# Performance work log

Hardware: AMD Instinct MI355X
Metric: run time of the kernel (lower is better)

The kernel has to match this reference:

```python
import jax, jax.numpy as jnp
import numpy as np

# Synthetic base image encoder: patchify(16) -> Linear(768,768)+ReLU -> Linear(768,3072)+ReLU -> mean-pool -> Linear(3072,512)
B, T = 32, 8          # batch, num task vectors
D, DH, F, MH = 768, 3072, 512, 128  # patch dim, hidden, feat_dim, meta-net hidden


def _patchify(x):
    # x: [B,3,224,224] -> [B,196,768] (14x14 patches of 16x16x3)
    Bn = x.shape[0]
    p = x.reshape(Bn, 3, 14, 16, 14, 16).transpose(0, 2, 4, 1, 3, 5)
    return p.reshape(Bn, 196, 768)


def _encode_shared(p, W1, b1, W2, b2, W3, b3):
    h = jax.nn.relu(p @ W1 + b1)          # [B,196,768]
    h2 = jax.nn.relu(h @ W2 + b2)         # [B,196,3072]
    return h2.mean(axis=1) @ W3 + b3      # [B,512]


def setup_inputs() -> dict:
    key = jax.random.key(0)
    ks = jax.random.split(key, 18)
    inp = {"x": jax.random.normal(ks[0], (B, 3, 224, 224), jnp.float32)}
    shapes = {
        "W1": (D, D), "b1": (D,), "W2": (D, DH), "b2": (DH,), "W3": (DH, F), "b3": (F,),
        "dW1": (T, D, D), "db1": (T, D), "dW2": (T, D, DH), "db2": (T, DH),
        "dW3": (T, DH, F), "db3": (T, F),
        "mW1": (F, MH), "mb1": (MH,), "mW2": (MH, T), "mb2": (T,),
    }
    for i, (n, sh) in enumerate(shapes.items()):
        inp[n] = jax.random.normal(ks[i + 1], sh, jnp.float32) * 0.02
    return inp


def reference(x, W1, b1, W2, b2, W3, b3, dW1, db1, dW2, db2, dW3, db3, mW1, mb1, mW2, mb2):
    p = _patchify(x)
    # base features computed with frozen params (torch.no_grad -> stop_gradient)
    base = jax.lax.stop_gradient(_encode_shared(p, W1, b1, W2, b2, W3, b3))
    # MetaNet: Linear-ReLU-Linear -> per-sample task-vector coefficients [B,T]
    coefs = jax.nn.relu(base @ mW1 + mb1) @ mW2 + mb2
    # per-sample composed parameters: theta_b = theta + sum_t coef[b,t] * dtheta_t
    W1b = W1 + jnp.einsum('bt,tde->bde', coefs, dW1)   # [B,768,768]
    b1b = b1 + coefs @ db1
    W2b = W2 + jnp.einsum('bt,tde->bde', coefs, dW2)   # [B,768,3072]
    b2b = b2 + coefs @ db2
    W3b = W3 + jnp.einsum('bt,tdf->bdf', coefs, dW3)   # [B,3072,512]
    b3b = b3 + coefs @ db3
    # batched per-sample forward (replaces the python loop over the batch)
    h = jax.nn.relu(jnp.einsum('bpd,bde->bpe', p, W1b) + b1b[:, None, :])
    h2 = jax.nn.relu(jnp.einsum('bpe,bef->bpf', h, W2b) + b2b[:, None, :])
    return jnp.einsum('be,bef->bf', h2.mean(axis=1), W3b) + b3b  # [B,512]
```

## Files before the change

### kernel.cpp

```cpp
#include <hip/hip_runtime.h>
#include <hip/hip_bf16.h>

#define BATCH 32
#define NPATCH 196
#define PD 768
#define DH 3072
#define FD 512
#define MH 128
#define NT 8

typedef unsigned short u16;
typedef u16   u16x8  __attribute__((ext_vector_type(8)));
typedef short bf16x8 __attribute__((ext_vector_type(8)));
typedef float f32x4  __attribute__((ext_vector_type(4)));

__device__ __forceinline__ void async16(const void* g, void* l)
{
    __builtin_amdgcn_global_load_lds(
        (const __attribute__((address_space(1))) void*)g,
        (__attribute__((address_space(3))) void*)l, 16, 0, 0);
}

#define BARRIER() do { asm volatile("" ::: "memory"); __builtin_amdgcn_s_barrier(); asm volatile("" ::: "memory"); } while (0)
#define VMWAIT(n) asm volatile("s_waitcnt vmcnt(" #n ")" ::: "memory")

#define GK  768
#define NK  24
#define GBM 256
#define GBN 128
#define GBK 32
#define ASZ (GBM*GBK)
#define BSZ (GBN*GBK)

__global__ __launch_bounds__(512, 4)
void gemm_bf16(const u16* __restrict__ A, const u16* __restrict__ BT,
               const float* __restrict__ bias, u16* __restrict__ C,
               float* __restrict__ pooled,
               int M, int N, long sA, long sB, long sC, long sBias,
               int relu, int pool)
{
    const int z = blockIdx.z;
    A  += (long)z * sA;
    BT += (long)z * sB;
    C  += (long)z * sC;
    const float* bz = bias ? bias + (long)z * sBias : nullptr;

    __shared__ __align__(16) u16 As[3 * ASZ];
    __shared__ __align__(16) u16 Bs[3 * BSZ];

    const int tid  = threadIdx.x;
    const int lane = tid & 63;
    const int wave = tid >> 6;
    const int wr = (wave >> 1) * 64;
    const int wc = (wave & 1) * 64;
    const int m0 = blockIdx.y * GBM;
    const int n0 = blockIdx.x * GBN;
    const int lrow = lane & 15;
    const int koff = (lane >> 4) * 8;

    f32x4 acc[4][4] = {};

    auto issue = [&](int kt, int bi) {
        u16* asb = As + bi * ASZ;
        u16* bsb = Bs + bi * BSZ;
        const int k0 = kt * GBK;
#pragma unroll
        for (int r = 0; r < 2; ++r) {
            int chunk = r * 512 + tid;
            int row = chunk >> 2;
            int k8  = chunk & 3;
            int gm  = m0 + row; if (gm >= M) gm = M - 1;
            async16(A + (long)gm * GK + k0 + k8 * 8,
                    asb + (size_t)(r * 512 + wave * 64) * 8);
        }
        int rowb = tid >> 2;
        int k8b  = tid & 3;
        async16(BT + (long)(n0 + rowb) * GK + k0 + k8b * 8,
                bsb + (size_t)(wave * 64) * 8);
    };

    auto compute = [&](int bi) {
        const u16* asb = As + bi * ASZ;
        const u16* bsb = Bs + bi * BSZ;
        bf16x8 af[4], bfr[4];
#pragma unroll
        for (int i = 0; i < 4; ++i)
            af[i] = *(const bf16x8*)(asb + (wr + i * 16 + lrow) * GBK + koff);
#pragma unroll
        for (int j = 0; j < 4; ++j)
            bfr[j] = *(const bf16x8*)(bsb + (wc + j * 16 + lrow) * GBK + koff);
#pragma unroll
        for (int i = 0; i < 4; ++i)
#pragma unroll
            for (int j = 0; j < 4; ++j)
                acc[i][j] = __builtin_amdgcn_mfma_f32_16x16x32_bf16(af[i], bfr[j], acc[i][j], 0, 0, 0);
    };

    issue(0, 0); issue(1, 1); issue(2, 2);

    for (int ii = 0; ii < 7; ++ii) {
        int i0 = ii * 3;
        VMWAIT(6); BARRIER(); compute(0); BARRIER(); issue(i0 + 3, 0);
        VMWAIT(6); BARRIER(); compute(1); BARRIER(); issue(i0 + 4, 1);
        VMWAIT(6); BARRIER(); compute(2); BARRIER(); issue(i0 + 5, 2);
    }
    VMWAIT(6); BARRIER(); compute(0); BARRIER();
    VMWAIT(3); BARRIER(); compute(1); BARRIER();
    VMWAIT(0); BARRIER(); compute(2);

    const int crow = (lane >> 4) * 4;
    const int ccol = lane & 15;

    if (!pool) {
#pragma unroll
        for (int j = 0; j < 4; ++j) {
            int gn = n0 + wc + j * 16 + ccol;
            float bv = bz ? bz[gn] : 0.f;
#pragma unroll
            for (int i = 0; i < 4; ++i) {
#pragma unroll
                for (int rg = 0; rg < 4; ++rg) {
                    int gm = m0 + wr + i * 16 + crow + rg;
                    if (gm < M) {
                        float v = acc[i][j][rg] + bv;
                        if (relu) v = fmaxf(v, 0.f);
                        __hip_bfloat16 hv = __float2bfloat16(v);
                        C[(long)gm * N + gn] = *(u16*)&hv;
                    }
                }
            }
        }
    } else {
        float* poolbuf = (float*)As;
        __syncthreads();
        const int slot = (wave >> 1) * 4 + (lane >> 4);
#pragma unroll
        for (int j = 0; j < 4; ++j) {
            int gn = n0 + wc + j * 16 + ccol;
            float bv = bz ? bz[gn] : 0.f;
            float s = 0.f;
#pragma unroll
            for (int i = 0; i < 4; ++i) {
#pragma unroll
                for (int rg = 0; rg < 4; ++rg) {
                    int gm = wr + i * 16 + crow + rg;
                    if (gm < NPATCH) s += fmaxf(acc[i][j][rg] + bv, 0.f);
                }
            }
            poolbuf[slot * 128 + wc + j * 16 + ccol] = s;
        }
        __syncthreads();
        if (tid < 128) {
            float s = 0.f;
#pragma unroll
            for (int q = 0; q < 16; ++q) s += poolbuf[q * 128 + tid];
            pooled[(long)z * N + n0 + tid] = s * (1.0f / NPATCH);
        }
    }
}

#define SK_KC  64
#define SK_PAD 36

__global__ __launch_bounds__(256)
void skinny3(const float* __restrict__ A, const float* __restrict__ B0,
             const float* __restrict__ dB, const float* __restrict__ cf,
             float* __restrict__ partial)
{
    const int ks = blockIdx.x;
    const int z  = blockIdx.y;
    const int KS = gridDim.x;
    const int k0 = ks * SK_KC;
    const float* B = (z == 0) ? B0 : dB + (long)(z - 1) * DH * FD;

    __shared__ __align__(16) float Asl[SK_KC][SK_PAD];

    const int tid  = threadIdx.x;
    const int nthr = tid & 63;
    const int bg   = tid >> 6;
    const int n    = nthr * 8;

    for (int idx = tid; idx < 32 * SK_KC; idx += 256) {
        int b = idx >> 6;
        int k = idx & (SK_KC - 1);
        float sc = (z == 0) ? 1.f : cf[b * NT + (z - 1)];
        Asl[k][b] = sc * A[(long)b * DH + k0 + k];
    }
    __syncthreads();

    f32x4 acc[8][2] = {};
    for (int k = 0; k < SK_KC; ++k) {
        const float* bp = B + (long)(k0 + k) * FD + n;
        f32x4 w0 = *(const f32x4*)bp;
        f32x4 w1 = *(const f32x4*)(bp + 4);
        f32x4 a0 = *(const f32x4*)&Asl[k][bg * 8];
        f32x4 a1 = *(const f32x4*)&Asl[k][bg * 8 + 4];
#pragma unroll
        for (int q = 0; q < 4; ++q) {
#pragma unroll
            for (int c = 0; c < 4; ++c) {
                acc[q][0][c]     = fmaf(a0[q], w0[c], acc[q][0][c]);
                acc[q][1][c]     = fmaf(a0[q], w1[c], acc[q][1][c]);
                acc[4 + q][0][c] = fmaf(a1[q], w0[c], acc[4 + q][0][c]);
                acc[4 + q][1][c] = fmaf(a1[q], w1[c], acc[4 + q][1][c]);
            }
        }
    }
    float* P = partial + ((long)(z * KS + ks) * BATCH + bg * 8) * FD + n;
#pragma unroll
    for (int bb = 0; bb < 8; ++bb) {
        *(f32x4*)(P + (long)bb * FD)     = acc[bb][0];
        *(f32x4*)(P + (long)bb * FD + 4) = acc[bb][1];
    }
}

__global__ __launch_bounds__(256)
void reduce_partials(const float* __restrict__ partial, float* __restrict__ dst, int per)
{
    int i  = blockIdx.x * 256 + threadIdx.x;
    int p0 = blockIdx.y * per;
    float s = 0.f;
    for (int p = 0; p < per; ++p)
        s += partial[(long)(p0 + p) * (BATCH * FD) + i];
    atomicAdd(&dst[i], s);
}

__global__ void patchify_bf(const float* __restrict__ x, u16* __restrict__ p, int total)
{
    int i = blockIdx.x * blockDim.x + threadIdx.x;
    if (i >= total) return;
    int d = i % PD;
    int rest = i / PD;
    int patch = rest % NPATCH;
    int b = rest / NPATCH;
    int c = d >> 8;
    int r = (d >> 4) & 15;
    int s = d & 15;
    int pr = patch / 14;
    int pc = patch % 14;
    float v = x[((long)(b * 3 + c) * 224 + (pr * 16 + r)) * 224 + (pc * 16 + s)];
    __hip_bfloat16 hv = __float2bfloat16(v);
    p[i] = *(u16*)&hv;
}

__global__ __launch_bounds__(256)
void wtrans2(const float* __restrict__ W1, u16* __restrict__ o1,
             const float* __restrict__ W2, u16* __restrict__ o2)
{
    const float* W; u16* outp; int K, N, t;
    if (blockIdx.x < 576) { W = W1; outp = o1; K = PD; N = PD;  t = blockIdx.x; }
    else                  { W = W2; outp = o2; K = PD; N = DH;  t = blockIdx.x - 576; }
    int nt = N / 32;
    int k0 = (t / nt) * 32;
    int n0 = (t % nt) * 32;

    __shared__ float Ws[32][33];
    const int tid = threadIdx.x;
#pragma unroll
    for (int r = 0; r < 4; ++r) {
        int idx = tid + r * 256;
        int kk = idx >> 5, nn = idx & 31;
        Ws[kk][nn] = W[(long)(k0 + kk) * N + n0 + nn];
    }
    __syncthreads();
#pragma unroll
    for (int r = 0; r < 4; ++r) {
        int idx = tid + r * 256;
        int kk = idx & 31, nn = idx >> 5;
        __hip_bfloat16 hv = __float2bfloat16(Ws[kk][nn]);
        outp[(long)(n0 + nn) * K + k0 + kk] = *(u16*)&hv;
    }
}

__global__ __launch_bounds__(128)
void compose_w(const float* __restrict__ W, const float* __restrict__ dW,
               const float* __restrict__ cf, u16* __restrict__ out,
               int K, int N)
{
    __shared__ float Ws[9][32][32];
    const int tid = threadIdx.x;
    const int k0 = blockIdx.x * 32;
    const int n0 = blockIdx.y * 32;
    const long tKN = (long)K * N;

#pragma unroll
    for (int a = 0; a < 9; ++a) {
        const float* src = (a == 0) ? W : dW + (long)(a - 1) * tKN;
#pragma unroll
        for (int r = 0; r < 8; ++r) {
            int idx = tid + r * 128;
            int kk = idx >> 5, nn = idx & 31;
            Ws[a][kk][nn] = src[(long)(k0 + kk) * N + n0 + nn];
        }
    }
    __syncthreads();

    const int nn = tid >> 2;
    const int k8 = (tid & 3) * 8;
    float w0[8], d[NT][8];
#pragma unroll
    for (int q = 0; q < 8; ++q) w0[q] = Ws[0][k8 + q][nn];
#pragma unroll
    for (int t = 0; t < NT; ++t)
#pragma unroll
        for (int q = 0; q < 8; ++q) d[t][q] = Ws[t + 1][k8 + q][nn];

    for (int b = 0; b < BATCH; ++b) {
        float c8[NT];
#pragma unroll
        for (int t = 0; t < NT; ++t) c8[t] = cf[b * NT + t];
        u16x8 o;
#pragma unroll
        for (int q = 0; q < 8; ++q) {
            float v = w0[q];
#pragma unroll
            for (int t = 0; t < NT; ++t) v = fmaf(c8[t], d[t][q], v);
            __hip_bfloat16 hv = __float2bfloat16(v);
            o[q] = *(u16*)&hv;
        }
        *(u16x8*)(out + ((long)b * N + (n0 + nn)) * K + k0 + k8) = o;
    }
}

__global__ void compose_bias3(const float* __restrict__ b1, const float* __restrict__ db1,
                              const float* __restrict__ b2, const float* __restrict__ db2,
                              const float* __restrict__ b3, const float* __restrict__ db3,
                              const float* __restrict__ cf,
                              float* __restrict__ o1, float* __restrict__ o2,
                              float* __restrict__ o3)
{
    int i = blockIdx.x * blockDim.x + threadIdx.x;
    const int t1 = BATCH * PD, t2 = BATCH * (PD + DH);
    const float* bs; const float* db; float* o; int N, j;
    if (i < t1)      { bs = b1; db = db1; o = o1; N = PD; j = i; }
    else if (i < t2) { bs = b2; db = db2; o = o2; N = DH; j = i - t1; }
    else {
        j = i - t2;
        if (j >= BATCH * FD) return;
        bs = b3; db = db3; o = o3; N = FD;
    }
    int n = j % N, b = j / N;
    float v = bs[n];
#pragma unroll
    for (int t = 0; t < NT; ++t) v = fmaf(cf[b * NT + t], db[(long)t * N + n], v);
    o[j] = v;
}

__global__ void bias_init(const float* __restrict__ bsrc, float* __restrict__ out, int N)
{
    int i = blockIdx.x * blockDim.x + threadIdx.x;
    if (i >= BATCH * N) return;
    out[i] = bsrc[i % N];
}

__global__ __launch_bounds__(256)
void hid_kernel(const float* __restrict__ base, const float* __restrict__ mW1,
                const float* __restrict__ mb1, float* __restrict__ hid)
{
    int gw   = blockIdx.x * 4 + (threadIdx.x >> 6);
    int lane = threadIdx.x & 63;
    int b = gw >> 7;
    int n = gw & 127;
    float s = 0.f;
#pragma unroll
    for (int i = 0; i < FD / 64; ++i) {
        int k = i * 64 + lane;
        s = fmaf(base[b * FD + k], mW1[k * MH + n], s);
    }
#pragma unroll
    for (int off = 32; off; off >>= 1) s += __shfl_down(s, off, 64);
    if (lane == 0) hid[gw] = fmaxf(s + mb1[n], 0.f);
}

__global__ void coef_kernel(const float* __restrict__ hidden, const float* __restrict__ mW2,
                            const float* __restrict__ mb2, float* __restrict__ coefs)
{
    int i = threadIdx.x;
    int t = i & 7;
    int b = i >> 3;
    float s = mb2[t];
    for (int k = 0; k < MH; ++k)
        s = fmaf(hidden[b * MH + k], mW2[k * NT + t], s);
    coefs[i] = s;
}

extern "C" void kernel_launch(void* const* d_in, const int* in_sizes, int n_in,
                              void* d_out, int out_size, void* d_ws, size_t ws_size,
                              hipStream_t stream)
{
    const float* x   = (const float*)d_in[0];
    const float* W1  = (const float*)d_in[1];
    const float* b1  = (const float*)d_in[2];
    const float* W2  = (const float*)d_in[3];
    const float* b2  = (const float*)d_in[4];
    const float* W3  = (const float*)d_in[5];
    const float* b3  = (const float*)d_in[6];
    const float* dW1 = (const float*)d_in[7];
    const float* db1 = (const float*)d_in[8];
    const float* dW2 = (const float*)d_in[9];
    const float* db2 = (const float*)d_in[10];
    const float* dW3 = (const float*)d_in[11];
    const float* db3 = (const float*)d_in[12];
    const float* mW1 = (const float*)d_in[13];
    const float* mb1 = (const float*)d_in[14];
    const float* mW2 = (const float*)d_in[15];
    const float* mb2 = (const float*)d_in[16];
    float* out = (float*)d_out;
    (void)n_in; (void)in_sizes; (void)out_size; (void)ws_size;

    char* w = (char*)d_ws;
    auto carve = [&](size_t bytes) { void* q = (void*)w; w += (bytes + 255) & ~(size_t)255; return q; };
    const int M1 = BATCH * NPATCH;
    const int KSPLITS = DH / SK_KC;

    u16*  p_bf  = (u16*)carve((size_t)M1 * PD * 2);
    u16*  h_bf  = (u16*)carve((size_t)M1 * PD * 2);
    u16*  W1T   = (u16*)carve((size_t)PD * PD * 2);
    u16*  W2T   = (u16*)carve((size_t)PD * DH * 2);
    u16*  W1bT  = (u16*)carve((size_t)BATCH * PD * PD * 2);
    u16*  W2bT  = (u16*)carve((size_t)BATCH * DH * PD * 2);
    float* b1b  = (float*)carve((size_t)BATCH * PD * 4);
    float* b2b  = (float*)carve((size_t)BATCH * DH * 4);
    float* h2m  = (float*)carve((size_t)BATCH * DH * 4);
    float* h2m2 = (float*)carve((size_t)BATCH * DH * 4);
    float* base = (float*)carve((size_t)BATCH * FD * 4);
    float* hid  = (float*)carve((size_t)BATCH * MH * 4);
    float* cf   = (float*)carve((size_t)BATCH * NT * 4);
    float* part = (float*)carve((size_t)9 * KSPLITS * BATCH * FD * 4);

    {
        int total = M1 * PD;
        patchify_bf<<<(total + 255) / 256, 256, 0, stream>>>(x, p_bf, total);
    }
    wtrans2<<<2880, 256, 0, stream>>>(W1, W1T, W2, W2T);
    gemm_bf16<<<dim3(PD / GBN, 25, 1), 512, 0, stream>>>(
        p_bf, W1T, b1, h_bf, nullptr, M1, PD, 0, 0, 0, 0, 1, 0);
    gemm_bf16<<<dim3(DH / GBN, 1, BATCH), 512, 0, stream>>>(
        h_bf, W2T, b2, nullptr, h2m, NPATCH, DH,
        (long)NPATCH * PD, 0, 0, 0, 1, 1);
    bias_init<<<(BATCH * FD + 255) / 256, 256, 0, stream>>>(b3, base, FD);
    skinny3<<<dim3(KSPLITS, 1), 256, 0, stream>>>(h2m, W3, nullptr, nullptr, part);
    reduce_partials<<<dim3(BATCH * FD / 256, 8), 256, 0, stream>>>(part, base, KSPLITS / 8);
    hid_kernel<<<BATCH * MH / 4, 256, 0, stream>>>(base, mW1, mb1, hid);
    coef_kernel<<<1, 256, 0, stream>>>(hid, mW2, mb2, cf);
    compose_w<<<dim3(PD / 32, PD / 32), 128, 0, stream>>>(W1, dW1, cf, W1bT, PD, PD);
    compose_w<<<dim3(PD / 32, DH / 32), 128, 0, stream>>>(W2, dW2, cf, W2bT, PD, DH);
    compose_bias3<<<(BATCH * (PD + DH + FD) + 255) / 256, 256, 0, stream>>>(
        b1, db1, b2, db2, b3, db3, cf, b1b, b2b, out);
    gemm_bf16<<<dim3(PD / GBN, 1, BATCH), 512, 0, stream>>>(
        p_bf, W1bT, b1b, h_bf, nullptr, NPATCH, PD,
        (long)NPATCH * PD, (long)PD * PD, (long)NPATCH * PD, PD, 1, 0);
    gemm_bf16<<<dim3(DH / GBN, 1, BATCH), 512, 0, stream>>>(
        h_bf, W2bT, b2b, nullptr, h2m2, NPATCH, DH,
        (long)NPATCH * PD, (long)DH * PD, 0, DH, 1, 1);
    skinny3<<<dim3(KSPLITS, 9), 256, 0, stream>>>(h2m2, W3, dW3, cf, part);
    reduce_partials<<<dim3(BATCH * FD / 256, 8), 256, 0, stream>>>(part, out, 9 * KSPLITS / 8);
}
```

Measured before the change: 521.6 us.

## Pre-tile GEMM B operands into contiguous K-blocks and fuse bias into partial reduction

Weight matrices are now written by the transpose and compose kernels in a tiled layout, with each 128-column by 32-K block stored contiguously, so the GEMM B loads become one linear 16-byte stream per thread. compose_w switches to 256 threads with vectorized float4 loads and 4-wide bf16 stores. reduce_partials becomes a single pass that folds the composed b3 bias in directly, replacing atomics and removing the bias_init kernel and the b3 part of compose_bias. The risks are that the layout is hardcoded for K=768, and that the reduction now has fewer blocks with a longer serial loop.

```diff
diff --git a/kernel.cpp b/kernel.cpp
--- a/kernel.cpp
+++ b/kernel.cpp
@@ -11,6 +11,7 @@
 
 typedef unsigned short u16;
 typedef u16   u16x8  __attribute__((ext_vector_type(8)));
+typedef u16   u16x4  __attribute__((ext_vector_type(4)));
 typedef short bf16x8 __attribute__((ext_vector_type(8)));
 typedef float f32x4  __attribute__((ext_vector_type(4)));
 
@@ -24,8 +25,8 @@
 #define BARRIER() do { asm volatile("" ::: "memory"); __builtin_amdgcn_s_barrier(); asm volatile("" ::: "memory"); } while (0)
 #define VMWAIT(n) asm volatile("s_waitcnt vmcnt(" #n ")" ::: "memory")
 
+
 #define GK  768
-#define NK  24
 #define GBM 256
 #define GBN 128
 #define GBK 32
@@ -58,6 +59,8 @@
     const int lrow = lane & 15;
     const int koff = (lane >> 4) * 8;
 
+    const u16* Bnt = BT + (size_t)(n0 >> 7) * 24 * 4096;
+
     f32x4 acc[4][4] = {};
 
     auto issue = [&](int kt, int bi) {
@@ -73,9 +76,7 @@
             async16(A + (long)gm * GK + k0 + k8 * 8,
                     asb + (size_t)(r * 512 + wave * 64) * 8);
         }
-        int rowb = tid >> 2;
-        int k8b  = tid & 3;
-        async16(BT + (long)(n0 + rowb) * GK + k0 + k8b * 8,
+        async16(Bnt + (size_t)kt * 4096 + (size_t)tid * 8,
                 bsb + (size_t)(wave * 64) * 8);
     };
 
@@ -215,14 +216,22 @@
 }
 
 __global__ __launch_bounds__(256)
-void reduce_partials(const float* __restrict__ partial, float* __restrict__ dst, int per)
-{
-    int i  = blockIdx.x * 256 + threadIdx.x;
-    int p0 = blockIdx.y * per;
-    float s = 0.f;
-    for (int p = 0; p < per; ++p)
-        s += partial[(long)(p0 + p) * (BATCH * FD) + i];
-    atomicAdd(&dst[i], s);
+void reduce_partials(const float* __restrict__ partial,
+                     const float* __restrict__ bias, const float* __restrict__ db,
+                     const float* __restrict__ cf,
+                     float* __restrict__ dst, int count)
+{
+    int i = blockIdx.x * 256 + threadIdx.x;
+    int f = i & (FD - 1);
+    int b = i >> 9;
+    float s = bias[f];
+    if (db) {
+#pragma unroll
+        for (int t = 0; t < NT; ++t) s = fmaf(cf[b * NT + t], db[t * FD + f], s);
+    }
+    for (int p = 0; p < count; ++p)
+        s += partial[(long)p * (BATCH * FD) + i];
+    dst[i] = s;
 }
 
 __global__ void patchify_bf(const float* __restrict__ x, u16* __restrict__ p, int total)
@@ -247,9 +256,9 @@
 void wtrans2(const float* __restrict__ W1, u16* __restrict__ o1,
              const float* __restrict__ W2, u16* __restrict__ o2)
 {
-    const float* W; u16* outp; int K, N, t;
-    if (blockIdx.x < 576) { W = W1; outp = o1; K = PD; N = PD;  t = blockIdx.x; }
-    else                  { W = W2; outp = o2; K = PD; N = DH;  t = blockIdx.x - 576; }
+    const float* W; u16* outp; int N, t;
+    if (blockIdx.x < 576) { W = W1; outp = o1; N = PD;  t = blockIdx.x; }
+    else                  { W = W2; outp = o2; N = DH;  t = blockIdx.x - 576; }
     int nt = N / 32;
     int k0 = (t / nt) * 32;
     int n0 = (t % nt) * 32;
@@ -263,94 +272,88 @@
         Ws[kk][nn] = W[(long)(k0 + kk) * N + n0 + nn];
     }
     __syncthreads();
+    u16* obase = outp + ((size_t)(n0 >> 7) * 24 + (k0 >> 5)) * 4096 + (size_t)(n0 & 127) * 32;
 #pragma unroll
     for (int r = 0; r < 4; ++r) {
         int idx = tid + r * 256;
         int kk = idx & 31, nn = idx >> 5;
         __hip_bfloat16 hv = __float2bfloat16(Ws[kk][nn]);
-        outp[(long)(n0 + nn) * K + k0 + kk] = *(u16*)&hv;
-    }
-}
-
-__global__ __launch_bounds__(128)
+        obase[nn * 32 + kk] = *(u16*)&hv;
+    }
+}
+
+__global__ __launch_bounds__(256)
 void compose_w(const float* __restrict__ W, const float* __restrict__ dW,
                const float* __restrict__ cf, u16* __restrict__ out,
-               int K, int N)
+               int N)
 {
     __shared__ float Ws[9][32][32];
     const int tid = threadIdx.x;
     const int k0 = blockIdx.x * 32;
     const int n0 = blockIdx.y * 32;
-    const long tKN = (long)K * N;
-
-#pragma unroll
-    for (int a = 0; a < 9; ++a) {
-        const float* src = (a == 0) ? W : dW + (long)(a - 1) * tKN;
-#pragma unroll
-        for (int r = 0; r < 8; ++r) {
-            int idx = tid + r * 128;
-            int kk = idx >> 5, nn = idx & 31;
-            Ws[a][kk][nn] = src[(long)(k0 + kk) * N + n0 + nn];
+    const long tKN = (long)GK * N;
+    const long bstride = (long)N * GK;
+
+    {
+        int kk  = tid >> 3;
+        int nn4 = (tid & 7) * 4;
+#pragma unroll
+        for (int a = 0; a < 9; ++a) {
+            const float* src = (a == 0) ? W : dW + (long)(a - 1) * tKN;
+            f32x4 v = *(const f32x4*)(src + (long)(k0 + kk) * N + n0 + nn4);
+            *(f32x4*)&Ws[a][kk][nn4] = v;
         }
     }
     __syncthreads();
 
-    const int nn = tid >> 2;
-    const int k8 = (tid & 3) * 8;
-    float w0[8], d[NT][8];
-#pragma unroll
-    for (int q = 0; q < 8; ++q) w0[q] = Ws[0][k8 + q][nn];
+    const int nn = tid >> 3;
+    const int k4 = (tid & 7) * 4;
+    float w0[4], d[NT][4];
+#pragma unroll
+    for (int q = 0; q < 4; ++q) w0[q] = Ws[0][k4 + q][nn];
 #pragma unroll
     for (int t = 0; t < NT; ++t)
 #pragma unroll
-        for (int q = 0; q < 8; ++q) d[t][q] = Ws[t + 1][k8 + q][nn];
-
+        for (int q = 0; q < 4; ++q) d[t][q] = Ws[t + 1][k4 + q][nn];
+
+    u16* obase = out + ((size_t)(n0 >> 7) * 24 + (k0 >> 5)) * 4096
+                     + (size_t)((n0 & 127) + nn) * 32 + k4;
     for (int b = 0; b < BATCH; ++b) {
         float c8[NT];
 #pragma unroll
         for (int t = 0; t < NT; ++t) c8[t] = cf[b * NT + t];
-        u16x8 o;
-#pragma unroll
-        for (int q = 0; q < 8; ++q) {
+        u16x4 o;
+#pragma unroll
+        for (int q = 0; q < 4; ++q) {
             float v = w0[q];
 #pragma unroll
             for (int t = 0; t < NT; ++t) v = fmaf(c8[t], d[t][q], v);
             __hip_bfloat16 hv = __float2bfloat16(v);
             o[q] = *(u16*)&hv;
         }
-        *(u16x8*)(out + ((long)b * N + (n0 + nn)) * K + k0 + k8) = o;
-    }
-}
-
-__global__ void compose_bias3(const float* __restrict__ b1, const float* __restrict__ db1,
+        *(u16x4*)(obase + (long)b * bstride) = o;
+    }
+}
+
+__global__ void compose_bias2(const float* __restrict__ b1, const float* __restrict__ db1,
                               const float* __restrict__ b2, const float* __restrict__ db2,
-                              const float* __restrict__ b3, const float* __restrict__ db3,
                               const float* __restrict__ cf,
-                              float* __restrict__ o1, float* __restrict__ o2,
-                              float* __restrict__ o3)
+                              float* __restrict__ o1, float* __restrict__ o2)
 {
     int i = blockIdx.x * blockDim.x + threadIdx.x;
-    const int t1 = BATCH * PD, t2 = BATCH * (PD + DH);
+    const int t1 = BATCH * PD;
     const float* bs; const float* db; float* o; int N, j;
-    if (i < t1)      { bs = b1; db = db1; o = o1; N = PD; j = i; }
-    else if (i < t2) { bs = b2; db = db2; o = o2; N = DH; j = i - t1; }
+    if (i < t1) { bs = b1; db = db1; o = o1; N = PD; j = i; }
     else {
-        j = i - t2;
-        if (j >= BATCH * FD) return;
-        bs = b3; db = db3; o = o3; N = FD;
+        j = i - t1;
+        if (j >= BATCH * DH) return;
+        bs = b2; db = db2; o = o2; N = DH;
     }
     int n = j % N, b = j / N;
     float v = bs[n];
 #pragma unroll
     for (int t = 0; t < NT; ++t) v = fmaf(cf[b * NT + t], db[(long)t * N + n], v);
     o[j] = v;
-}
-
-__global__ void bias_init(const float* __restrict__ bsrc, float* __restrict__ out, int N)
-{
-    int i = blockIdx.x * blockDim.x + threadIdx.x;
-    if (i >= BATCH * N) return;
-    out[i] = bsrc[i % N];
 }
 
 __global__ __launch_bounds__(256)
@@ -438,15 +441,14 @@
     gemm_bf16<<<dim3(DH / GBN, 1, BATCH), 512, 0, stream>>>(
         h_bf, W2T, b2, nullptr, h2m, NPATCH, DH,
         (long)NPATCH * PD, 0, 0, 0, 1, 1);
-    bias_init<<<(BATCH * FD + 255) / 256, 256, 0, stream>>>(b3, base, FD);
     skinny3<<<dim3(KSPLITS, 1), 256, 0, stream>>>(h2m, W3, nullptr, nullptr, part);
-    reduce_partials<<<dim3(BATCH * FD / 256, 8), 256, 0, stream>>>(part, base, KSPLITS / 8);
+    reduce_partials<<<BATCH * FD / 256, 256, 0, stream>>>(part, b3, nullptr, nullptr, base, KSPLITS);
     hid_kernel<<<BATCH * MH / 4, 256, 0, stream>>>(base, mW1, mb1, hid);
     coef_kernel<<<1, 256, 0, stream>>>(hid, mW2, mb2, cf);
-    compose_w<<<dim3(PD / 32, PD / 32), 128, 0, stream>>>(W1, dW1, cf, W1bT, PD, PD);
-    compose_w<<<dim3(PD / 32, DH / 32), 128, 0, stream>>>(W2, dW2, cf, W2bT, PD, DH);
-    compose_bias3<<<(BATCH * (PD + DH + FD) + 255) / 256, 256, 0, stream>>>(
-        b1, db1, b2, db2, b3, db3, cf, b1b, b2b, out);
+    compose_w<<<dim3(24, PD / 32), 256, 0, stream>>>(W1, dW1, cf, W1bT, PD);
+    compose_w<<<dim3(24, DH / 32), 256, 0, stream>>>(W2, dW2, cf, W2bT, DH);
+    compose_bias2<<<(BATCH * (PD + DH) + 255) / 256, 256, 0, stream>>>(
+        b1, db1, b2, db2, cf, b1b, b2b);
     gemm_bf16<<<dim3(PD / GBN, 1, BATCH), 512, 0, stream>>>(
         p_bf, W1bT, b1b, h_bf, nullptr, NPATCH, PD,
         (long)NPATCH * PD, (long)PD * PD, (long)NPATCH * PD, PD, 1, 0);
@@ -454,5 +456,5 @@
         h_bf, W2bT, b2b, nullptr, h2m2, NPATCH, DH,
         (long)NPATCH * PD, (long)DH * PD, 0, DH, 1, 1);
     skinny3<<<dim3(KSPLITS, 9), 256, 0, stream>>>(h2m2, W3, dW3, cf, part);
-    reduce_partials<<<dim3(BATCH * FD / 256, 8), 256, 0, stream>>>(part, out, 9 * KSPLITS / 8);
-}
+    reduce_partials<<<BATCH * FD / 256, 256, 0, stream>>>(part, b3, db3, cf, out, 9 * KSPLITS);
+}
```

Result: slower. 591.9 us (+13.5%).
